# Kernel optimization log

Hardware: AMD Instinct MI355X
Metric: run time of the kernel (lower is better)

Reference implementation:

```python
import jax, jax.numpy as jnp
import numpy as np

MIN_C = 1e-5   # base_c * DYNAMIC_CURVATURE_MIN_RATIO
MAX_C = 10.0   # base_c * DYNAMIC_CURVATURE_MAX_RATIO
T = 0.7
EPS = 1e-7
B, IN_DIM, HID, OUT_DIM = 4096, 4096, 4096, 1024


def _artanh(x):
    x = jnp.clip(x, -1.0 + 1e-5, 1.0 - 1e-5)
    return 0.5 * jnp.log1p(2.0 * x / (1.0 - x))


def _mobius_scalar_mul(r, x, c):
    # r: python float, x: [B,D], c: [B,1] per-row curvature
    sqrt_c = jnp.sqrt(c)
    norm = jnp.clip(jnp.linalg.norm(x, axis=-1, keepdims=True), EPS)
    arg = jnp.clip(sqrt_c * norm, EPS, 1.0 - 1e-5)
    return jnp.tanh(r * _artanh(arg)) * x / (sqrt_c * norm)


def _mobius_add(x, y, c):
    xy = jnp.sum(x * y, axis=-1, keepdims=True)
    x2 = jnp.sum(x * x, axis=-1, keepdims=True)
    y2 = jnp.sum(y * y, axis=-1, keepdims=True)
    num = (1.0 + 2.0 * c * xy + c * y2) * x + (1.0 - c * x2) * y
    den = 1.0 + 2.0 * c * xy + c * c * x2 * y2
    return num / jnp.clip(den, EPS)


def poincare_ball_layer(h, u, c, t):
    # geodesic-style layer: ((1-t) (*) h) (+) (t (*) u) on the Poincare ball
    return _mobius_add(_mobius_scalar_mul(1.0 - t, h, c),
                       _mobius_scalar_mul(t, u, c), c)


def setup_inputs() -> dict:
    key = jax.random.key(0)
    ks = jax.random.split(key, 8)
    std = 0.02  # WEIGHT_INIT_STD_IMPROVED
    return {
        "x": jax.random.normal(ks[0], (B, IN_DIM), jnp.float32),
        "W1": jax.random.normal(ks[1], (IN_DIM, HID), jnp.float32) * std,
        "b1": jnp.zeros((HID,), jnp.float32),
        "W2": jax.random.normal(ks[2], (HID, HID), jnp.float32) * std,
        "b2": jnp.zeros((HID,), jnp.float32),
        "Wout": jax.random.normal(ks[3], (HID, OUT_DIM), jnp.float32) * std,
        "bout": jnp.zeros((OUT_DIM,), jnp.float32),
        "curv_feat": jax.random.normal(ks[4], (16,), jnp.float32) * 0.01,
        "curv_scale": jnp.ones((1,), jnp.float32) * 0.1,
        "proj": jax.random.normal(ks[5], (IN_DIM, 16), jnp.float32),
    }


def reference(x, W1, b1, W2, b2, Wout, bout, curv_feat, curv_scale, proj):
    x_flat = x.reshape(x.shape[0], -1)
    h = jnp.tanh(x_flat @ W1 + b1)            # [B, HID]
    u = jax.nn.sigmoid(h @ W2 + b2)           # [B, HID]
    # adaptive curvature prediction (vectorized over batch)
    x_red = x_flat @ proj                     # [B, 16]
    feat_inter = x_red @ curv_feat            # [B]
    adj = jax.nn.sigmoid(feat_inter + curv_scale[0])
    c = MIN_C + (MAX_C - MIN_C) * adj         # [B]
    c = jnp.clip(c, MIN_C, MAX_C)[:, None]    # [B, 1]
    z = poincare_ball_layer(h, u, c, T)
    # NaN fallback per row (mirrors torch per-sample isnan check)
    z = jnp.where(jnp.any(jnp.isnan(z), axis=1, keepdims=True), h, z)
    return z @ Wout + bout
```

## Files before the change

kernel.cpp:

```cpp
#include <hip/hip_runtime.h>
#include <hip/hip_bf16.h>
#include <math.h>


typedef __attribute__((ext_vector_type(8))) __bf16 bf16x8;
typedef __attribute__((ext_vector_type(4))) float  f32x4;

constexpr int BATCH = 4096;
constexpr int IND   = 4096;
constexpr int HIDD  = 4096;
constexpr int OUTD  = 1024;
constexpr float T_C  = 0.7f;
constexpr float MINC = 1e-5f;
constexpr float MAXC = 10.0f;
constexpr float EPSV = 1e-7f;

__device__ __forceinline__ float bf2f(unsigned int us) {
    return __uint_as_float(us << 16);
}
__device__ __forceinline__ unsigned short f2bf(float f) {
    unsigned int u = __float_as_uint(f);
    u = (u + 0x7FFFu + ((u >> 16) & 1u)) >> 16;
    return (unsigned short)u;
}

__global__ __launch_bounds__(256)
void cast_curv(const float* __restrict__ x, const float* __restrict__ v,
               const float* __restrict__ cs,
               unsigned short* __restrict__ xb, float* __restrict__ c)
{
    const int row = blockIdx.x;
    const float* xr = x + (size_t)row * IND;
    unsigned short* ob = xb + (size_t)row * IND;
    float s = 0.f;
    for (int i = threadIdx.x; i < IND / 4; i += 256) {
        float4 w  = ((const float4*)xr)[i];
        float4 vv = ((const float4*)v)[i];
        s += w.x * vv.x + w.y * vv.y + w.z * vv.z + w.w * vv.w;
        ushort4 o;
        o.x = f2bf(w.x); o.y = f2bf(w.y); o.z = f2bf(w.z); o.w = f2bf(w.w);
        ((ushort4*)ob)[i] = o;
    }
    #pragma unroll
    for (int o = 32; o > 0; o >>= 1) s += __shfl_down(s, o, 64);
    __shared__ float red[4];
    if ((threadIdx.x & 63) == 0) red[threadIdx.x >> 6] = s;
    __syncthreads();
    if (threadIdx.x == 0) {
        float tot = red[0] + red[1] + red[2] + red[3];
        float adj = 1.0f / (1.0f + expf(-(tot + cs[0])));
        float cc  = MINC + (MAXC - MINC) * adj;
        c[row] = fminf(fmaxf(cc, MINC), MAXC);
    }
}

__global__ __launch_bounds__(256)
void transpose_cast(const float* __restrict__ in, unsigned short* __restrict__ out,
                    int K, int N)
{
    __shared__ float tile[32][33];
    const int k0 = blockIdx.y * 32;
    const int n0 = blockIdx.x * 32;
    const int t = threadIdx.x;
    #pragma unroll
    for (int i = 0; i < 4; i++) {
        int idx = t + i * 256;
        int r = idx >> 5, c = idx & 31;
        tile[r][c] = in[(size_t)(k0 + r) * N + n0 + c];
    }
    __syncthreads();
    #pragma unroll
    for (int i = 0; i < 4; i++) {
        int idx = t + i * 256;
        int r = idx >> 5, c = idx & 31;
        out[(size_t)(n0 + r) * K + k0 + c] = f2bf(tile[c][r]);
    }
}

template<int EPI>
__global__ __launch_bounds__(512)
void gemm256(const unsigned short* __restrict__ A,
             const unsigned short* __restrict__ Bt,
             const float* __restrict__ bias,
             unsigned short* __restrict__ outp,
             int N, int K)
{
    __shared__ unsigned short lds[4 * 256 * 64];
    unsigned short* Al = lds;
    unsigned short* Bl = lds + 2 * 256 * 64;

    const int t = threadIdx.x;
    const int w = t >> 6, l = t & 63;
    const int wr = w >> 2, wc = w & 3;
    const int lr = l & 15, lg = l >> 4;

    const int nwg = gridDim.x * gridDim.y;
    const int bid = blockIdx.y * gridDim.x + blockIdx.x;
    const int q8 = nwg >> 3, r8 = nwg & 7;
    const int xcd = bid & 7, off = bid >> 3;
    const int wgid = (xcd < r8 ? xcd * (q8 + 1) : r8 * (q8 + 1) + (xcd - r8) * q8) + off;
    const int by = wgid / gridDim.x;
    const int bx = wgid % gridDim.x;

    const int row0 = by * 256, col0 = bx * 256;
    const unsigned short* Ab = A  + (size_t)row0 * K;
    const unsigned short* Bb = Bt + (size_t)col0 * K;
    const int NT = K >> 6;

    f32x4 acc[8][4] = {};

    auto stage_half = [&](int kt, int buf, int mat, int h) {
        const int kb = kt * 128;
        const unsigned short* gb = mat ? Bb : Ab;
        unsigned short* lb = (mat ? Bl : Al) + buf * 16384 + h * 8192;
        #pragma unroll
        for (int qq = 0; qq < 2; qq++) {
            const int id  = qq * 512 + t;
            const int row = h * 128 + (id >> 3);
            const int cb  = (id & 7) * 16;
            const int scb = cb ^ ((row & 7) << 4);
            const char* src = (const char*)gb + (size_t)row * ((size_t)K * 2) + kb + scb;
            __builtin_amdgcn_global_load_lds(
                (const __attribute__((address_space(1))) unsigned int*)src,
                (__attribute__((address_space(3))) unsigned int*)(lb + id * 8), 16, 0, 0);
        }
    };

    stage_half(0, 0, 0, 0);
    stage_half(0, 0, 1, 0);
    stage_half(0, 0, 1, 1);
    stage_half(0, 0, 0, 1);
    asm volatile("s_waitcnt vmcnt(2)" ::: "memory");
    __builtin_amdgcn_s_barrier();

    const int sw = (lr & 7) << 4;
    const int c0 = (lg * 16) ^ sw;
    const int c1 = (64 + lg * 16) ^ sw;

    for (int kt = 0; kt < NT; ++kt) {
        const int buf = kt & 1, nb = buf ^ 1;
        const bool pre = (kt + 1 < NT);
        const char* AlB = (const char*)Al + buf * 32768 + (wr * 16 + lr) * 128;
        const char* BlB = (const char*)Bl + buf * 32768 + (wc * 64 + lr) * 128;

        bf16x8 bfk[4], afk[4];

        #pragma unroll
        for (int ni = 0; ni < 4; ni++) bfk[ni] = *(const bf16x8*)(BlB + ni * 2048 + c0);
        #pragma unroll
        for (int mi = 0; mi < 4; mi++) afk[mi] = *(const bf16x8*)(AlB + mi * 4096 + c0);
        if (pre) { stage_half(kt + 1, nb, 0, 0); stage_half(kt + 1, nb, 1, 0); }
        __builtin_amdgcn_s_setprio(1);
        #pragma unroll
        for (int mi = 0; mi < 4; mi++)
            #pragma unroll
            for (int ni = 0; ni < 4; ni++)
                acc[mi][ni] = __builtin_amdgcn_mfma_f32_16x16x32_bf16(
                    afk[mi], bfk[ni], acc[mi][ni], 0, 0, 0);
        __builtin_amdgcn_s_setprio(0);
        if (pre) asm volatile("s_waitcnt vmcnt(4)" ::: "memory");
        else     asm volatile("s_waitcnt vmcnt(0)" ::: "memory");
        __builtin_amdgcn_s_barrier();

        #pragma unroll
        for (int mi = 0; mi < 4; mi++) afk[mi] = *(const bf16x8*)(AlB + (4 + mi) * 4096 + c0);
        if (pre) { stage_half(kt + 1, nb, 1, 1); stage_half(kt + 1, nb, 0, 1); }
        __builtin_amdgcn_s_setprio(1);
        #pragma unroll
        for (int mi = 0; mi < 4; mi++)
            #pragma unroll
            for (int ni = 0; ni < 4; ni++)
                acc[4 + mi][ni] = __builtin_amdgcn_mfma_f32_16x16x32_bf16(
                    afk[mi], bfk[ni], acc[4 + mi][ni], 0, 0, 0);
        __builtin_amdgcn_s_setprio(0);
        __builtin_amdgcn_s_barrier();

        #pragma unroll
        for (int ni = 0; ni < 4; ni++) bfk[ni] = *(const bf16x8*)(BlB + ni * 2048 + c1);
        #pragma unroll
        for (int mi = 0; mi < 4; mi++) afk[mi] = *(const bf16x8*)(AlB + mi * 4096 + c1);
        __builtin_amdgcn_s_setprio(1);
        #pragma unroll
        for (int mi = 0; mi < 4; mi++)
            #pragma unroll
            for (int ni = 0; ni < 4; ni++)
                acc[mi][ni] = __builtin_amdgcn_mfma_f32_16x16x32_bf16(
                    afk[mi], bfk[ni], acc[mi][ni], 0, 0, 0);
        __builtin_amdgcn_s_setprio(0);
        __builtin_amdgcn_s_barrier();

        #pragma unroll
        for (int mi = 0; mi < 4; mi++) afk[mi] = *(const bf16x8*)(AlB + (4 + mi) * 4096 + c1);
        __builtin_amdgcn_s_setprio(1);
        #pragma unroll
        for (int mi = 0; mi < 4; mi++)
            #pragma unroll
            for (int ni = 0; ni < 4; ni++)
                acc[4 + mi][ni] = __builtin_amdgcn_mfma_f32_16x16x32_bf16(
                    afk[mi], bfk[ni], acc[4 + mi][ni], 0, 0, 0);
        __builtin_amdgcn_s_setprio(0);
        if (pre) asm volatile("s_waitcnt vmcnt(2)" ::: "memory");
        else     asm volatile("s_waitcnt vmcnt(0)" ::: "memory");
        __builtin_amdgcn_s_barrier();
    }

    const int colb = col0 + wc * 64;
    #pragma unroll
    for (int ni = 0; ni < 4; ni++) {
        const int cg = colb + ni * 16 + lr;
        const float bv = bias[cg];
        #pragma unroll
        for (int mi = 0; mi < 8; mi++) {
            #pragma unroll
            for (int r = 0; r < 4; r++) {
                const int rg = row0 + wr * 16 + mi * 32 + lg * 4 + r;
                float v = acc[mi][ni][r] + bv;
                if constexpr (EPI == 0) v = tanhf(v);
                else                    v = 1.0f / (1.0f + expf(-v));
                outp[(size_t)rg * N + cg] = f2bf(v);
            }
        }
    }
}

__global__ __launch_bounds__(256)
void gemm_bt_f32(const unsigned short* __restrict__ A,
                 const unsigned short* __restrict__ Bt,
                 const float* __restrict__ bias,
                 float* __restrict__ outp,
                 int N, int K)
{
    __shared__ unsigned short Asl[128 * 32];
    __shared__ unsigned short Bsl[128 * 32];

    const int t  = threadIdx.x;
    const int w  = t >> 6, l = t & 63;
    const int wr = w >> 1, wc = w & 1;
    const int row0 = blockIdx.y * 128;
    const int col0 = blockIdx.x * 128;

    const unsigned short* Ab = A  + (size_t)row0 * K;
    const unsigned short* Bb = Bt + (size_t)col0 * K;

    const int lr = l & 15;
    const int lk = (l >> 4) * 8;

    f32x4 acc[4][4] = {};

    for (int k0 = 0; k0 < K; k0 += 32) {
        __syncthreads();
        #pragma unroll
        for (int q = 0; q < 2; q++) {
            int idx = q * 256 + t;
            int r   = idx >> 2;
            int c8  = (idx & 3) * 8;
            __builtin_amdgcn_global_load_lds(
                (const __attribute__((address_space(1))) unsigned int*)(Ab + (size_t)r * K + k0 + c8),
                (__attribute__((address_space(3))) unsigned int*)(&Asl[idx * 8]), 16, 0, 0);
            __builtin_amdgcn_global_load_lds(
                (const __attribute__((address_space(1))) unsigned int*)(Bb + (size_t)r * K + k0 + c8),
                (__attribute__((address_space(3))) unsigned int*)(&Bsl[idx * 8]), 16, 0, 0);
        }
        __syncthreads();

        bf16x8 af[4], bfr[4];
        #pragma unroll
        for (int mi = 0; mi < 4; mi++)
            af[mi] = *(const bf16x8*)(&Asl[(wr * 64 + mi * 16 + lr) * 32 + lk]);
        #pragma unroll
        for (int ni = 0; ni < 4; ni++)
            bfr[ni] = *(const bf16x8*)(&Bsl[(wc * 64 + ni * 16 + lr) * 32 + lk]);

        #pragma unroll
        for (int mi = 0; mi < 4; mi++)
            #pragma unroll
            for (int ni = 0; ni < 4; ni++)
                acc[mi][ni] = __builtin_amdgcn_mfma_f32_16x16x32_bf16(
                    af[mi], bfr[ni], acc[mi][ni], 0, 0, 0);
    }

    const int colb = col0 + wc * 64;
    const int rowb = row0 + wr * 64 + (l >> 4) * 4;
    #pragma unroll
    for (int ni = 0; ni < 4; ni++) {
        const int cg = colb + ni * 16 + lr;
        const float bv = bias[cg];
        #pragma unroll
        for (int mi = 0; mi < 4; mi++)
            #pragma unroll
            for (int r = 0; r < 4; r++)
                outp[(size_t)(rowb + mi * 16 + r) * N + cg] = acc[mi][ni][r] + bv;
    }
}

__global__ __launch_bounds__(256)
void proj_cf(const float* __restrict__ proj, const float* __restrict__ cf,
             float* __restrict__ v)
{
    int i = blockIdx.x * 256 + threadIdx.x;
    if (i < IND) {
        float s = 0.f;
        #pragma unroll
        for (int j = 0; j < 16; j++) s += proj[i * 16 + j] * cf[j];
        v[i] = s;
    }
}

__global__ __launch_bounds__(256)
void poincare_kernel(const unsigned short* __restrict__ hb,
                     const unsigned short* __restrict__ ub,
                     const float* __restrict__ c,
                     unsigned short* __restrict__ zb)
{
    const int row = blockIdx.x;
    const int t = threadIdx.x;
    const size_t base = (size_t)row * HIDD;

    float hv[16], uv[16];
    float h2 = 0.f, u2 = 0.f, hu = 0.f;
    #pragma unroll
    for (int q = 0; q < 2; q++) {
        const int e0 = (q * 256 + t) * 8;
        uint4 hc = *(const uint4*)(hb + base + e0);
        uint4 uc = *(const uint4*)(ub + base + e0);
        const unsigned int hw[4] = {hc.x, hc.y, hc.z, hc.w};
        const unsigned int uw[4] = {uc.x, uc.y, uc.z, uc.w};
        #pragma unroll
        for (int i = 0; i < 4; i++) {
            float h0 = bf2f(hw[i] & 0xFFFFu), h1 = bf2f(hw[i] >> 16);
            float u0 = bf2f(uw[i] & 0xFFFFu), u1 = bf2f(uw[i] >> 16);
            hv[q * 8 + 2 * i]     = h0; hv[q * 8 + 2 * i + 1] = h1;
            uv[q * 8 + 2 * i]     = u0; uv[q * 8 + 2 * i + 1] = u1;
            h2 += h0 * h0 + h1 * h1;
            u2 += u0 * u0 + u1 * u1;
            hu += h0 * u0 + h1 * u1;
        }
    }
    #pragma unroll
    for (int o = 32; o > 0; o >>= 1) {
        h2 += __shfl_down(h2, o, 64);
        u2 += __shfl_down(u2, o, 64);
        hu += __shfl_down(hu, o, 64);
    }
    __shared__ float red[3][4];
    const int w = t >> 6;
    if ((t & 63) == 0) { red[0][w] = h2; red[1][w] = u2; red[2][w] = hu; }
    __syncthreads();
    h2 = red[0][0] + red[0][1] + red[0][2] + red[0][3];
    u2 = red[1][0] + red[1][1] + red[1][2] + red[1][3];
    hu = red[2][0] + red[2][1] + red[2][2] + red[2][3];

    const float cc = c[row];
    const float sc = sqrtf(cc);
    float nh = fmaxf(sqrtf(h2), EPSV);
    float nu = fmaxf(sqrtf(u2), EPSV);
    float ah = fminf(fmaxf(sc * nh, EPSV), 1.0f - 1e-5f);
    float au = fminf(fmaxf(sc * nu, EPSV), 1.0f - 1e-5f);
    float ath = 0.5f * log1pf(2.0f * ah / (1.0f - ah));
    float atu = 0.5f * log1pf(2.0f * au / (1.0f - au));
    float alpha = tanhf((1.0f - T_C) * ath) / (sc * nh);
    float beta  = tanhf(T_C * atu) / (sc * nu);
    float x2 = alpha * alpha * h2;
    float y2 = beta * beta * u2;
    float xy = alpha * beta * hu;
    float den = 1.0f + 2.0f * cc * xy + cc * cc * x2 * y2;
    den = fmaxf(den, EPSV);
    float ca = (1.0f + 2.0f * cc * xy + cc * y2) * alpha / den;
    float cb = (1.0f - cc * x2) * beta / den;
    if (isnan(ca) || isnan(cb)) { ca = 1.0f; cb = 0.0f; }

    #pragma unroll
    for (int q = 0; q < 2; q++) {
        const int e0 = (q * 256 + t) * 8;
        unsigned int ow[4];
        #pragma unroll
        for (int i = 0; i < 4; i++) {
            float z0 = ca * hv[q * 8 + 2 * i]     + cb * uv[q * 8 + 2 * i];
            float z1 = ca * hv[q * 8 + 2 * i + 1] + cb * uv[q * 8 + 2 * i + 1];
            ow[i] = (unsigned int)f2bf(z0) | ((unsigned int)f2bf(z1) << 16);
        }
        *(uint4*)(zb + base + e0) = make_uint4(ow[0], ow[1], ow[2], ow[3]);
    }
}

extern "C" void kernel_launch(void* const* d_in, const int* in_sizes, int n_in,
                              void* d_out, int out_size, void* d_ws, size_t ws_size,
                              hipStream_t stream)
{
    const float* x    = (const float*)d_in[0];
    const float* W1   = (const float*)d_in[1];
    const float* b1   = (const float*)d_in[2];
    const float* W2   = (const float*)d_in[3];
    const float* b2   = (const float*)d_in[4];
    const float* Wout = (const float*)d_in[5];
    const float* bout = (const float*)d_in[6];
    const float* cf   = (const float*)d_in[7];
    const float* cs   = (const float*)d_in[8];
    const float* proj = (const float*)d_in[9];
    float* out = (float*)d_out;

    char* ws = (char*)d_ws;
    unsigned short* x_bf = (unsigned short*)(ws);
    unsigned short* w_bf = (unsigned short*)(ws + (33554432));
    unsigned short* h_bf = (unsigned short*)(ws + (67108864));
    unsigned short* u_bf = (unsigned short*)(ws + (100663296));
    float* vvec = (float*)(ws + 134217728);
    float* cvec = (float*)(ws + 134217728 + 16384);

    proj_cf<<<IND / 256, 256, 0, stream>>>(proj, cf, vvec);
    cast_curv<<<BATCH, 256, 0, stream>>>(x, vvec, cs, x_bf, cvec);

    transpose_cast<<<dim3(HIDD / 32, IND / 32), 256, 0, stream>>>(W1, w_bf, IND, HIDD);
    gemm256<0><<<dim3(HIDD / 256, BATCH / 256), 512, 0, stream>>>(x_bf, w_bf, b1, h_bf, HIDD, IND);

    transpose_cast<<<dim3(HIDD / 32, HIDD / 32), 256, 0, stream>>>(W2, w_bf, HIDD, HIDD);
    gemm256<1><<<dim3(HIDD / 256, BATCH / 256), 512, 0, stream>>>(h_bf, w_bf, b2, u_bf, HIDD, HIDD);

    poincare_kernel<<<BATCH, 256, 0, stream>>>(h_bf, u_bf, cvec, x_bf);

    transpose_cast<<<dim3(OUTD / 32, HIDD / 32), 256, 0, stream>>>(Wout, w_bf, HIDD, OUTD);
    gemm_bt_f32<<<dim3(OUTD / 128, BATCH / 128), 256, 0, stream>>>(x_bf, w_bf, bout, out, OUTD, HIDD);
}
```

Measured before the change: 434.9 us.

## Pipeline output GEMM, vectorize weight transpose, precompute staging addresses in main GEMM

```diff
diff --git a/kernel.cpp b/kernel.cpp
--- a/kernel.cpp
+++ b/kernel.cpp
@@ -5,6 +5,7 @@
 
 typedef __attribute__((ext_vector_type(8))) __bf16 bf16x8;
 typedef __attribute__((ext_vector_type(4))) float  f32x4;
+typedef __attribute__((ext_vector_type(8))) unsigned short us8;
 
 constexpr int BATCH = 4096;
 constexpr int IND   = 4096;
@@ -22,6 +23,11 @@
     unsigned int u = __float_as_uint(f);
     u = (u + 0x7FFFu + ((u >> 16) & 1u)) >> 16;
     return (unsigned short)u;
+}
+__device__ __forceinline__ void stage16(const char* src, unsigned short* dst) {
+    __builtin_amdgcn_global_load_lds(
+        (const __attribute__((address_space(1))) unsigned int*)src,
+        (__attribute__((address_space(3))) unsigned int*)dst, 16, 0, 0);
 }
 
 __global__ __launch_bounds__(256)
@@ -55,30 +61,35 @@
 }
 
 __global__ __launch_bounds__(256)
-void transpose_cast(const float* __restrict__ in, unsigned short* __restrict__ out,
-                    int K, int N)
-{
-    __shared__ float tile[32][33];
-    const int k0 = blockIdx.y * 32;
-    const int n0 = blockIdx.x * 32;
+void transpose_cast64(const float* __restrict__ in, unsigned short* __restrict__ out,
+                      int K, int N)
+{
+    __shared__ float tile[64][65];
+    const int k0 = blockIdx.y * 64;
+    const int n0 = blockIdx.x * 64;
     const int t = threadIdx.x;
     #pragma unroll
     for (int i = 0; i < 4; i++) {
-        int idx = t + i * 256;
-        int r = idx >> 5, c = idx & 31;
-        tile[r][c] = in[(size_t)(k0 + r) * N + n0 + c];
+        const int idx = i * 256 + t;
+        const int r = idx >> 4, c4 = (idx & 15) * 4;
+        float4 v = *(const float4*)(&in[(size_t)(k0 + r) * N + n0 + c4]);
+        tile[r][c4 + 0] = v.x; tile[r][c4 + 1] = v.y;
+        tile[r][c4 + 2] = v.z; tile[r][c4 + 3] = v.w;
     }
     __syncthreads();
     #pragma unroll
-    for (int i = 0; i < 4; i++) {
-        int idx = t + i * 256;
-        int r = idx >> 5, c = idx & 31;
-        out[(size_t)(n0 + r) * K + k0 + c] = f2bf(tile[c][r]);
+    for (int j = 0; j < 2; j++) {
+        const int idx = j * 256 + t;
+        const int r = idx >> 3, c8 = (idx & 7) * 8;
+        us8 o;
+        #pragma unroll
+        for (int e = 0; e < 8; e++) o[e] = f2bf(tile[c8 + e][r]);
+        *(us8*)(&out[(size_t)(n0 + r) * K + k0 + c8]) = o;
     }
 }
 
 template<int EPI>
-__global__ __launch_bounds__(512)
+__global__ __launch_bounds__(512, 2)
 void gemm256(const unsigned short* __restrict__ A,
              const unsigned short* __restrict__ Bt,
              const float* __restrict__ bias,
@@ -86,8 +97,6 @@
              int N, int K)
 {
     __shared__ unsigned short lds[4 * 256 * 64];
-    unsigned short* Al = lds;
-    unsigned short* Bl = lds + 2 * 256 * 64;
 
     const int t = threadIdx.x;
     const int w = t >> 6, l = t & 63;
@@ -109,47 +118,62 @@
 
     f32x4 acc[8][4] = {};
 
-    auto stage_half = [&](int kt, int buf, int mat, int h) {
-        const int kb = kt * 128;
-        const unsigned short* gb = mat ? Bb : Ab;
-        unsigned short* lb = (mat ? Bl : Al) + buf * 16384 + h * 8192;
-        #pragma unroll
-        for (int qq = 0; qq < 2; qq++) {
-            const int id  = qq * 512 + t;
-            const int row = h * 128 + (id >> 3);
-            const int cb  = (id & 7) * 16;
-            const int scb = cb ^ ((row & 7) << 4);
-            const char* src = (const char*)gb + (size_t)row * ((size_t)K * 2) + kb + scb;
-            __builtin_amdgcn_global_load_lds(
-                (const __attribute__((address_space(1))) unsigned int*)src,
-                (__attribute__((address_space(3))) unsigned int*)(lb + id * 8), 16, 0, 0);
-        }
-    };
-
-    stage_half(0, 0, 0, 0);
-    stage_half(0, 0, 1, 0);
-    stage_half(0, 0, 1, 1);
-    stage_half(0, 0, 0, 1);
-    asm volatile("s_waitcnt vmcnt(2)" ::: "memory");
-    __builtin_amdgcn_s_barrier();
+    const int id0 = t, id1 = 512 + t;
+    const int r0 = id0 >> 3, r1 = id1 >> 3;
+    const int cb0 = (id0 & 7) * 16, cb1 = (id1 & 7) * 16;
+    const int s0 = cb0 ^ ((r0 & 7) << 4), s1 = cb1 ^ ((r1 & 7) << 4);
+    const size_t K2 = (size_t)K * 2;
+    const char* pA00 = (const char*)Ab + (size_t)r0 * K2 + s0;
+    const char* pA01 = (const char*)Ab + (size_t)r1 * K2 + s1;
+    const char* pA10 = pA00 + 128 * K2;
+    const char* pA11 = pA01 + 128 * K2;
+    const char* pB00 = (const char*)Bb + (size_t)r0 * K2 + s0;
+    const char* pB01 = (const char*)Bb + (size_t)r1 * K2 + s1;
+    const char* pB10 = pB00 + 128 * K2;
+    const char* pB11 = pB01 + 128 * K2;
+    const int dA0a = id0 * 8,          dA0b = id1 * 8;
+    const int dA1a = 8192 + id0 * 8,   dA1b = 8192 + id1 * 8;
+    const int dB0a = 32768 + id0 * 8,  dB0b = 32768 + id1 * 8;
+    const int dB1a = 40960 + id0 * 8,  dB1b = 40960 + id1 * 8;
 
     const int sw = (lr & 7) << 4;
     const int c0 = (lg * 16) ^ sw;
     const int c1 = (64 + lg * 16) ^ sw;
+    const int aofc0 = (wr * 16 + lr) * 128 + c0;
+    const int aofc1 = (wr * 16 + lr) * 128 + c1;
+    const int bofc0 = 65536 + (wc * 64 + lr) * 128 + c0;
+    const int bofc1 = 65536 + (wc * 64 + lr) * 128 + c1;
+    const char* ldsb = (const char*)lds;
+
+    stage16(pA00, lds + dA0a); stage16(pA01, lds + dA0b);
+    stage16(pB00, lds + dB0a); stage16(pB01, lds + dB0b);
+    stage16(pB10, lds + dB1a); stage16(pB11, lds + dB1b);
+    stage16(pA10, lds + dA1a); stage16(pA11, lds + dA1b);
+    asm volatile("s_waitcnt vmcnt(2)" ::: "memory");
+    __builtin_amdgcn_s_barrier();
 
     for (int kt = 0; kt < NT; ++kt) {
         const int buf = kt & 1, nb = buf ^ 1;
         const bool pre = (kt + 1 < NT);
-        const char* AlB = (const char*)Al + buf * 32768 + (wr * 16 + lr) * 128;
-        const char* BlB = (const char*)Bl + buf * 32768 + (wc * 64 + lr) * 128;
+        pA00 += 128; pA01 += 128; pA10 += 128; pA11 += 128;
+        pB00 += 128; pB01 += 128; pB10 += 128; pB11 += 128;
+        const int bufby = buf * 32768;
+        const int bsh   = nb * 16384;
+        const char* rA0 = ldsb + bufby + aofc0;
+        const char* rA1 = ldsb + bufby + aofc1;
+        const char* rB0 = ldsb + bufby + bofc0;
+        const char* rB1 = ldsb + bufby + bofc1;
 
         bf16x8 bfk[4], afk[4];
 
         #pragma unroll
-        for (int ni = 0; ni < 4; ni++) bfk[ni] = *(const bf16x8*)(BlB + ni * 2048 + c0);
-        #pragma unroll
-        for (int mi = 0; mi < 4; mi++) afk[mi] = *(const bf16x8*)(AlB + mi * 4096 + c0);
-        if (pre) { stage_half(kt + 1, nb, 0, 0); stage_half(kt + 1, nb, 1, 0); }
+        for (int ni = 0; ni < 4; ni++) bfk[ni] = *(const bf16x8*)(rB0 + ni * 2048);
+        #pragma unroll
+        for (int mi = 0; mi < 4; mi++) afk[mi] = *(const bf16x8*)(rA0 + mi * 4096);
+        if (pre) {
+            stage16(pA00, lds + bsh + dA0a); stage16(pA01, lds + bsh + dA0b);
+            stage16(pB00, lds + bsh + dB0a); stage16(pB01, lds + bsh + dB0b);
+        }
         __builtin_amdgcn_s_setprio(1);
         #pragma unroll
         for (int mi = 0; mi < 4; mi++)
@@ -163,8 +187,11 @@
         __builtin_amdgcn_s_barrier();
 
         #pragma unroll
-        for (int mi = 0; mi < 4; mi++) afk[mi] = *(const bf16x8*)(AlB + (4 + mi) * 4096 + c0);
-        if (pre) { stage_half(kt + 1, nb, 1, 1); stage_half(kt + 1, nb, 0, 1); }
+        for (int mi = 0; mi < 4; mi++) afk[mi] = *(const bf16x8*)(rA0 + 16384 + mi * 4096);
+        if (pre) {
+            stage16(pB10, lds + bsh + dB1a); stage16(pB11, lds + bsh + dB1b);
+            stage16(pA10, lds + bsh + dA1a); stage16(pA11, lds + bsh + dA1b);
+        }
         __builtin_amdgcn_s_setprio(1);
         #pragma unroll
         for (int mi = 0; mi < 4; mi++)
@@ -176,9 +203,9 @@
         __builtin_amdgcn_s_barrier();
 
         #pragma unroll
-        for (int ni = 0; ni < 4; ni++) bfk[ni] = *(const bf16x8*)(BlB + ni * 2048 + c1);
-        #pragma unroll
-        for (int mi = 0; mi < 4; mi++) afk[mi] = *(const bf16x8*)(AlB + mi * 4096 + c1);
+        for (int ni = 0; ni < 4; ni++) bfk[ni] = *(const bf16x8*)(rB1 + ni * 2048);
+        #pragma unroll
+        for (int mi = 0; mi < 4; mi++) afk[mi] = *(const bf16x8*)(rA1 + mi * 4096);
         __builtin_amdgcn_s_setprio(1);
         #pragma unroll
         for (int mi = 0; mi < 4; mi++)
@@ -190,7 +217,7 @@
         __builtin_amdgcn_s_barrier();
 
         #pragma unroll
-        for (int mi = 0; mi < 4; mi++) afk[mi] = *(const bf16x8*)(AlB + (4 + mi) * 4096 + c1);
+        for (int mi = 0; mi < 4; mi++) afk[mi] = *(const bf16x8*)(rA1 + 16384 + mi * 4096);
         __builtin_amdgcn_s_setprio(1);
         #pragma unroll
         for (int mi = 0; mi < 4; mi++)
@@ -223,73 +250,114 @@
     }
 }
 
-__global__ __launch_bounds__(256)
-void gemm_bt_f32(const unsigned short* __restrict__ A,
+__global__ __launch_bounds__(512, 2)
+void gemm_out128(const unsigned short* __restrict__ A,
                  const unsigned short* __restrict__ Bt,
                  const float* __restrict__ bias,
                  float* __restrict__ outp,
                  int N, int K)
 {
-    __shared__ unsigned short Asl[128 * 32];
-    __shared__ unsigned short Bsl[128 * 32];
-
-    const int t  = threadIdx.x;
-    const int w  = t >> 6, l = t & 63;
-    const int wr = w >> 1, wc = w & 1;
-    const int row0 = blockIdx.y * 128;
-    const int col0 = blockIdx.x * 128;
-
+    __shared__ unsigned short lds[32768];
+
+    const int t = threadIdx.x;
+    const int w = t >> 6, l = t & 63;
+    const int wr = w >> 2, wc = w & 3;
+    const int lr = l & 15, lg = l >> 4;
+
+    const int nwg = gridDim.x * gridDim.y;
+    const int bid = blockIdx.y * gridDim.x + blockIdx.x;
+    const int q8 = nwg >> 3, r8 = nwg & 7;
+    const int xcd = bid & 7, off = bid >> 3;
+    const int wgid = (xcd < r8 ? xcd * (q8 + 1) : r8 * (q8 + 1) + (xcd - r8) * q8) + off;
+    const int by = wgid / gridDim.x;
+    const int bx = wgid % gridDim.x;
+
+    const int row0 = by * 128, col0 = bx * 128;
     const unsigned short* Ab = A  + (size_t)row0 * K;
     const unsigned short* Bb = Bt + (size_t)col0 * K;
-
-    const int lr = l & 15;
-    const int lk = (l >> 4) * 8;
-
-    f32x4 acc[4][4] = {};
-
-    for (int k0 = 0; k0 < K; k0 += 32) {
-        __syncthreads();
-        #pragma unroll
-        for (int q = 0; q < 2; q++) {
-            int idx = q * 256 + t;
-            int r   = idx >> 2;
-            int c8  = (idx & 3) * 8;
-            __builtin_amdgcn_global_load_lds(
-                (const __attribute__((address_space(1))) unsigned int*)(Ab + (size_t)r * K + k0 + c8),
-                (__attribute__((address_space(3))) unsigned int*)(&Asl[idx * 8]), 16, 0, 0);
-            __builtin_amdgcn_global_load_lds(
-                (const __attribute__((address_space(1))) unsigned int*)(Bb + (size_t)r * K + k0 + c8),
-                (__attribute__((address_space(3))) unsigned int*)(&Bsl[idx * 8]), 16, 0, 0);
-        }
-        __syncthreads();
-
-        bf16x8 af[4], bfr[4];
-        #pragma unroll
-        for (int mi = 0; mi < 4; mi++)
-            af[mi] = *(const bf16x8*)(&Asl[(wr * 64 + mi * 16 + lr) * 32 + lk]);
-        #pragma unroll
-        for (int ni = 0; ni < 4; ni++)
-            bfr[ni] = *(const bf16x8*)(&Bsl[(wc * 64 + ni * 16 + lr) * 32 + lk]);
-
-        #pragma unroll
-        for (int mi = 0; mi < 4; mi++)
-            #pragma unroll
-            for (int ni = 0; ni < 4; ni++)
-                acc[mi][ni] = __builtin_amdgcn_mfma_f32_16x16x32_bf16(
-                    af[mi], bfr[ni], acc[mi][ni], 0, 0, 0);
-    }
-
-    const int colb = col0 + wc * 64;
-    const int rowb = row0 + wr * 64 + (l >> 4) * 4;
-    #pragma unroll
-    for (int ni = 0; ni < 4; ni++) {
-        const int cg = colb + ni * 16 + lr;
+    const int NT = K >> 6;
+
+    f32x4 acc[4][2] = {};
+
+    const int sr = t >> 2;
+    const int scb = ((t & 3) * 16) ^ ((sr & 3) << 4);
+    const size_t K2 = (size_t)K * 2;
+    const char* pAk0 = (const char*)Ab + (size_t)sr * K2 + scb;
+    const char* pAk1 = pAk0 + 64;
+    const char* pBk0 = (const char*)Bb + (size_t)sr * K2 + scb;
+    const char* pBk1 = pBk0 + 64;
+    const int dAk0 = t * 8,          dAk1 = 4096 + t * 8;
+    const int dBk0 = 16384 + t * 8,  dBk1 = 20480 + t * 8;
+
+    const int csw = (lg * 16) ^ ((lr & 3) << 4);
+    const int aof = (wr * 64 + lr) * 64 + csw;
+    const int bof = 32768 + (wc * 32 + lr) * 64 + csw;
+    const char* ldsb = (const char*)lds;
+
+    stage16(pAk0, lds + dAk0); stage16(pBk0, lds + dBk0);
+    stage16(pAk1, lds + dAk1); stage16(pBk1, lds + dBk1);
+    asm volatile("s_waitcnt vmcnt(2)" ::: "memory");
+    __builtin_amdgcn_s_barrier();
+
+    for (int kt = 0; kt < NT; ++kt) {
+        const int buf = kt & 1, nb = buf ^ 1;
+        const bool pre = (kt + 1 < NT);
+        pAk0 += 128; pAk1 += 128; pBk0 += 128; pBk1 += 128;
+        const int bufby = buf * 16384;
+        const int bsh   = nb * 8192;
+        const char* rA0 = ldsb + bufby + aof;
+        const char* rB0 = ldsb + bufby + bof;
+        const char* rA1 = rA0 + 8192;
+        const char* rB1 = rB0 + 8192;
+
+        bf16x8 af[4], bfr[2];
+
+        #pragma unroll
+        for (int nj = 0; nj < 2; nj++) bfr[nj] = *(const bf16x8*)(rB0 + nj * 1024);
+        #pragma unroll
+        for (int mi = 0; mi < 4; mi++) af[mi] = *(const bf16x8*)(rA0 + mi * 1024);
+        if (pre) { stage16(pAk0, lds + bsh + dAk0); stage16(pBk0, lds + bsh + dBk0); }
+        __builtin_amdgcn_s_setprio(1);
+        #pragma unroll
+        for (int mi = 0; mi < 4; mi++)
+            #pragma unroll
+            for (int nj = 0; nj < 2; nj++)
+                acc[mi][nj] = __builtin_amdgcn_mfma_f32_16x16x32_bf16(
+                    af[mi], bfr[nj], acc[mi][nj], 0, 0, 0);
+        __builtin_amdgcn_s_setprio(0);
+        if (pre) asm volatile("s_waitcnt vmcnt(2)" ::: "memory");
+        else     asm volatile("s_waitcnt vmcnt(0)" ::: "memory");
+        __builtin_amdgcn_s_barrier();
+
+        #pragma unroll
+        for (int nj = 0; nj < 2; nj++) bfr[nj] = *(const bf16x8*)(rB1 + nj * 1024);
+        #pragma unroll
+        for (int mi = 0; mi < 4; mi++) af[mi] = *(const bf16x8*)(rA1 + mi * 1024);
+        if (pre) { stage16(pAk1, lds + bsh + dAk1); stage16(pBk1, lds + bsh + dBk1); }
+        __builtin_amdgcn_s_setprio(1);
+        #pragma unroll
+        for (int mi = 0; mi < 4; mi++)
+            #pragma unroll
+            for (int nj = 0; nj < 2; nj++)
+                acc[mi][nj] = __builtin_amdgcn_mfma_f32_16x16x32_bf16(
+                    af[mi], bfr[nj], acc[mi][nj], 0, 0, 0);
+        __builtin_amdgcn_s_setprio(0);
+        if (pre) asm volatile("s_waitcnt vmcnt(2)" ::: "memory");
+        else     asm volatile("s_waitcnt vmcnt(0)" ::: "memory");
+        __builtin_amdgcn_s_barrier();
+    }
+
+    #pragma unroll
+    for (int nj = 0; nj < 2; nj++) {
+        const int cg = col0 + wc * 32 + nj * 16 + lr;
         const float bv = bias[cg];
         #pragma unroll
         for (int mi = 0; mi < 4; mi++)
             #pragma unroll
-            for (int r = 0; r < 4; r++)
-                outp[(size_t)(rowb + mi * 16 + r) * N + cg] = acc[mi][ni][r] + bv;
+            for (int r = 0; r < 4; r++) {
+                const int rg = row0 + wr * 64 + mi * 16 + lg * 4 + r;
+                outp[(size_t)rg * N + cg] = acc[mi][nj][r] + bv;
+            }
     }
 }
 
@@ -410,14 +478,14 @@
     proj_cf<<<IND / 256, 256, 0, stream>>>(proj, cf, vvec);
     cast_curv<<<BATCH, 256, 0, stream>>>(x, vvec, cs, x_bf, cvec);
 
-    transpose_cast<<<dim3(HIDD / 32, IND / 32), 256, 0, stream>>>(W1, w_bf, IND, HIDD);
+    transpose_cast64<<<dim3(HIDD / 64, IND / 64), 256, 0, stream>>>(W1, w_bf, IND, HIDD);
     gemm256<0><<<dim3(HIDD / 256, BATCH / 256), 512, 0, stream>>>(x_bf, w_bf, b1, h_bf, HIDD, IND);
 
-    transpose_cast<<<dim3(HIDD / 32, HIDD / 32), 256, 0, stream>>>(W2, w_bf, HIDD, HIDD);
+    transpose_cast64<<<dim3(HIDD / 64, HIDD / 64), 256, 0, stream>>>(W2, w_bf, HIDD, HIDD);
     gemm256<1><<<dim3(HIDD / 256, BATCH / 256), 512, 0, stream>>>(h_bf, w_bf, b2, u_bf, HIDD, HIDD);
 
     poincare_kernel<<<BATCH, 256, 0, stream>>>(h_bf, u_bf, cvec, x_bf);
 
-    transpose_cast<<<dim3(OUTD / 32, HIDD / 32), 256, 0, stream>>>(Wout, w_bf, HIDD, OUTD);
-    gemm_bt_f32<<<dim3(OUTD / 128, BATCH / 128), 256, 0, stream>>>(x_bf, w_bf, bout, out, OUTD, HIDD);
-}
+    transpose_cast64<<<dim3(OUTD / 64, HIDD / 64), 256, 0, stream>>>(Wout, w_bf, HIDD, OUTD);
+    gemm_out128<<<dim3(OUTD / 128, BATCH / 128), 512, 0, stream>>>(x_bf, w_bf, bout, out, OUTD, HIDD);
+}
```

Measured after the change: 386.1 us. 11.2% less time.
